# Kernel tuning notes

Measured on AMD Instinct MI355X. Metric: run time of the kernel, lower is better.

Reference implementation:

```python
import jax, jax.numpy as jnp
import numpy as np

ALPHA = 50.0  # softmax temperature from __init__
EPS = 1e-12   # torch F.normalize eps


def _l2norm(v, axis):
    return v / jnp.maximum(jnp.linalg.norm(v, axis=axis, keepdims=True), EPS)


def setup_inputs() -> dict:
    key = jax.random.key(0)
    k1, k2 = jax.random.split(key)
    N, C, H, W, K = 64, 512, 32, 32, 64
    x = jax.random.normal(k1, (N, C, H, W), jnp.float32)
    # conv.weight after _init_params has shape (dim, num_clusters) = (C, K)
    conv_weight = jax.random.normal(k2, (C, K), jnp.float32) * 0.05
    conv_bias = jnp.zeros((K,), jnp.float32)
    return {"x": x, "conv_weight": conv_weight, "conv_bias": conv_bias}


def reference(x, conv_weight, conv_bias):
    N, C, H, W = x.shape
    HW = H * W
    # normalize_input=True: L2 normalize over channel dim
    xn = _l2norm(x, axis=1)
    xf = xn.reshape(N, C, HW)                      # [N, C, HW]
    # column-normalized projection weight (F.normalize(conv.weight, dim=0))
    Wn = _l2norm(conv_weight, axis=0)              # [C, K]
    # soft assignment logits: x^T Wn -> stored as [N, K, HW]
    sa_logits = jnp.einsum('nch,ck->nkh', xf, Wn)  # [N, K, HW]
    soft_assign = jax.nn.softmax((sa_logits + conv_bias[None, :, None]) * ALPHA, axis=1)
    # VLAD via two batched contractions instead of the [N,K,C,HW] residual tensor:
    # sum_h a[n,k,h] * (x[n,:,h] - W[:,k]) = (a @ x^T)[n,k,:] - (sum_h a) * W[:,k]
    vlad = jnp.einsum('nkh,nch->nkc', soft_assign, xf) \
         - soft_assign.sum(-1)[..., None] * conv_weight.T[None]   # [N, K, C]
    vlad = _l2norm(vlad, axis=2).reshape(N, -1)    # intra-norm + flatten -> [N, K*C]
    feature = jnp.transpose(xf, (0, 2, 1))         # [N, HW, C]
    return (vlad, sa_logits, feature)
```

## Files before the change

kernel.cpp:

```cpp
#include <hip/hip_runtime.h>
#include <math.h>

#define N_   64
#define C_   512
#define HW_  1024
#define K_   64
#define ALPHA_ 50.0f
#define EPS_  1e-12f

#define OUT_VLAD 0
#define OUT_SA   2097152
#define OUT_FEAT 6291456

#define WSB_WT    0
#define WSB_WNTB  131072
#define WSB_INVN  196608
#define WSB_A     458752
#define WSB_SUMA  8847360
#define WSB_PART  8863744
#define PART_ELEMS 2097152

typedef __attribute__((ext_vector_type(8))) __bf16 bf16x8;
typedef __attribute__((ext_vector_type(4))) float f32x4;
typedef __attribute__((ext_vector_type(8))) unsigned short ushort8v;

__device__ inline unsigned short f2bf(float f) {
    unsigned int u = __builtin_bit_cast(unsigned int, f);
    u = (u + 0x7FFFu + ((u >> 16) & 1u)) >> 16;
    return (unsigned short)u;
}
__device__ inline float bf2f(unsigned short h) {
    unsigned int u = ((unsigned int)h) << 16;
    return __builtin_bit_cast(float, u);
}
__device__ inline f32x4 mfma16(const unsigned short* pa, const unsigned short* pb, f32x4 c) {
    bf16x8 a = *(const bf16x8*)pa;
    bf16x8 b = *(const bf16x8*)pb;
    return __builtin_amdgcn_mfma_f32_16x16x32_bf16(a, b, c, 0, 0, 0);
}

__global__ __launch_bounds__(256) void k1_weights(const float* __restrict__ W,
                                                  float* __restrict__ wT,
                                                  unsigned short* __restrict__ wnTb) {
    int k = blockIdx.x;
    int t = threadIdx.x;
    __shared__ float red[256];
    float s = 0.f;
    for (int c = t; c < C_; c += 256) { float w = W[c * K_ + k]; s += w * w; }
    red[t] = s;
    __syncthreads();
    for (int st = 128; st > 0; st >>= 1) {
        if (t < st) red[t] += red[t + st];
        __syncthreads();
    }
    float inv = 1.f / fmaxf(sqrtf(red[0]), EPS_);
    for (int c = t; c < C_; c += 256) {
        float w = W[c * K_ + k];
        wT[k * C_ + c]   = w;
        wnTb[k * C_ + c] = f2bf(w * inv);
    }
}

__global__ __launch_bounds__(256) void k2_normfeat(const float* __restrict__ x,
                                                   float* __restrict__ out,
                                                   float* __restrict__ invn) {
    float* feat = out + OUT_FEAT;
    int b   = blockIdx.x;
    int n   = b >> 6;
    int hw0 = (b & 63) << 4;
    int t   = threadIdx.x;
    __shared__ float Xs[C_ * 17 + 256 + 16];
    float* red = Xs + C_ * 17;
    float* nrm = red + 256;
    const float* xn = x + (long)n * C_ * HW_;
    for (int j = 0; j < 32; ++j) {
        int idx = j * 256 + t;
        int c = idx >> 4, p = idx & 15;
        Xs[c * 17 + p] = xn[c * HW_ + hw0 + p];
    }
    __syncthreads();
    {
        int p = t & 15, cg = t >> 4;
        float s = 0.f;
        for (int j = 0; j < 32; ++j) {
            float v = Xs[(cg + 16 * j) * 17 + p];
            s += v * v;
        }
        red[t] = s;
    }
    __syncthreads();
    if (t < 16) {
        float s = 0.f;
        for (int g = 0; g < 16; ++g) s += red[g * 16 + t];
        float iv = 1.f / fmaxf(sqrtf(s), EPS_);
        nrm[t] = iv;
        invn[(long)n * HW_ + hw0 + t] = iv;
    }
    __syncthreads();
    float* frow = feat + ((long)n * HW_ + hw0) * C_;
    for (int p = 0; p < 16; ++p) {
        float iv = nrm[p];
        frow[(long)p * C_ + t]       = Xs[t * 17 + p] * iv;
        frow[(long)p * C_ + t + 256] = Xs[(t + 256) * 17 + p] * iv;
    }
}

#define K3PITCH 136
__global__ __launch_bounds__(256, 4) void k3_sa(const float* __restrict__ feat,
                                                const unsigned short* __restrict__ wnTb,
                                                const float* __restrict__ bias,
                                                float* __restrict__ sa,
                                                unsigned short* __restrict__ Ab) {
    __shared__ alignas(16) unsigned short sm[128 * K3PITCH + 64 * K3PITCH];
    unsigned short* Fsh = sm;
    unsigned short* Wsh = sm + 128 * K3PITCH;
    float* Ls = (float*)sm;
    float* Bz = Ls + 8448;
    float* Zm = Ls + 8512;
    float* Iv = Ls + 8640;

    int b   = blockIdx.x;
    int n   = b >> 3;
    int hw0 = (b & 7) << 7;
    int t   = threadIdx.x;
    int l   = t & 63, w = t >> 6;
    int mr  = l & 15, q = l >> 4;

    f32x4 acc[2][4];
#pragma unroll
    for (int i = 0; i < 2; ++i)
#pragma unroll
        for (int j = 0; j < 4; ++j) acc[i][j] = (f32x4){0.f, 0.f, 0.f, 0.f};

    const float* fb = feat + ((long)n * HW_ + hw0) * C_;
    for (int ch = 0; ch < 4; ++ch) {
        int c0 = ch * 128;
        __syncthreads();
#pragma unroll
        for (int j = 0; j < 8; ++j) {
            int idx = j * 256 + t;
            int row = idx >> 4, sg = idx & 15;
            const float* src = fb + (long)row * C_ + c0 + sg * 8;
            float4 v0 = *(const float4*)src;
            float4 v1 = *(const float4*)(src + 4);
            ushort8v pk;
            pk[0] = f2bf(v0.x); pk[1] = f2bf(v0.y); pk[2] = f2bf(v0.z); pk[3] = f2bf(v0.w);
            pk[4] = f2bf(v1.x); pk[5] = f2bf(v1.y); pk[6] = f2bf(v1.z); pk[7] = f2bf(v1.w);
            *(ushort8v*)(Fsh + row * K3PITCH + sg * 8) = pk;
        }
#pragma unroll
        for (int j = 0; j < 4; ++j) {
            int idx = j * 256 + t;
            int row = idx >> 4, sg = idx & 15;
            *(uint4*)(Wsh + row * K3PITCH + sg * 8) =
                *(const uint4*)(wnTb + row * C_ + c0 + sg * 8);
        }
        __syncthreads();
#pragma unroll
        for (int ks = 0; ks < 4; ++ks) {
            int ko = ks * 32 + q * 8;
            const unsigned short* ap0 = Fsh + (w * 32 + mr) * K3PITCH + ko;
            const unsigned short* ap1 = Fsh + (w * 32 + 16 + mr) * K3PITCH + ko;
#pragma unroll
            for (int j = 0; j < 4; ++j) {
                const unsigned short* bp = Wsh + (j * 16 + mr) * K3PITCH + ko;
                acc[0][j] = mfma16(ap0, bp, acc[0][j]);
                acc[1][j] = mfma16(ap1, bp, acc[1][j]);
            }
        }
    }
    __syncthreads();
#pragma unroll
    for (int i = 0; i < 2; ++i)
#pragma unroll
        for (int j = 0; j < 4; ++j)
#pragma unroll
            for (int r = 0; r < 4; ++r)
                Ls[(j * 16 + mr) * 132 + w * 32 + i * 16 + q * 4 + r] = acc[i][j][r];
    if (t < 64) Bz[t] = bias[t];
    __syncthreads();
    if (t < 128) {
        int p = t;
        float mx = -1e30f;
        for (int kc = 0; kc < 64; ++kc) {
            float z = (Ls[kc * 132 + p] + Bz[kc]) * ALPHA_;
            mx = fmaxf(mx, z);
        }
        float s = 0.f;
        for (int kc = 0; kc < 64; ++kc) {
            float z = (Ls[kc * 132 + p] + Bz[kc]) * ALPHA_;
            s += __expf(z - mx);
        }
        Zm[p] = mx;
        Iv[p] = 1.f / s;
    }
    __syncthreads();
    float* sab = sa + (long)n * K_ * HW_ + hw0;
    unsigned short* Arow = Ab + (long)n * K_ * HW_ + hw0;
#pragma unroll
    for (int j = 0; j < 32; ++j) {
        int idx = j * 256 + t;
        int kc = idx >> 7, p = idx & 127;
        float v = Ls[kc * 132 + p];
        sab[(long)kc * HW_ + p] = v;
        float z = (v + Bz[kc]) * ALPHA_;
        Arow[(long)kc * HW_ + p] = f2bf(__expf(z - Zm[p]) * Iv[p]);
    }
}

__global__ __launch_bounds__(256) void k3b_suma(const unsigned short* __restrict__ Ab,
                                                float* __restrict__ sumA) {
    int b = blockIdx.x, t = threadIdx.x;
    int wv = t >> 6, l = t & 63;
    int row = b * 4 + wv;
    const unsigned int* ar = (const unsigned int*)(Ab + (long)row * HW_);
    float s = 0.f;
#pragma unroll
    for (int i = 0; i < 8; ++i) {
        unsigned int u = ar[i * 64 + l];
        s += bf2f((unsigned short)(u & 0xFFFF)) + bf2f((unsigned short)(u >> 16));
    }
#pragma unroll
    for (int off = 32; off > 0; off >>= 1) s += __shfl_down(s, off, 64);
    if (l == 0) sumA[row] = s;
}

#define K4PITCH 72
__global__ __launch_bounds__(256, 4) void k4_vlad(const float* __restrict__ x,
                                                  const float* __restrict__ invn,
                                                  const unsigned short* __restrict__ Ab,
                                                  float* __restrict__ part) {
    __shared__ float invs[512];
    __shared__ alignas(16) unsigned short Ash[64 * K4PITCH];
    __shared__ alignas(16) unsigned short Fsh[128 * K4PITCH];
    int b  = blockIdx.x;
    int n  = b >> 3;
    int r  = b & 7;
    int ct = r & 3, hh = r >> 2;
    int c_off = ct * 128, h_base = hh * 512;
    int t = threadIdx.x;
    int l = t & 63, w = t >> 6;
    int mr = l & 15, q = l >> 4;
    int kcb = (w >> 1) * 32, cb = (w & 1) * 64;

    invs[t]       = invn[(long)n * HW_ + h_base + t];
    invs[t + 256] = invn[(long)n * HW_ + h_base + 256 + t];

    f32x4 acc[2][4];
#pragma unroll
    for (int i = 0; i < 2; ++i)
#pragma unroll
        for (int j = 0; j < 4; ++j) acc[i][j] = (f32x4){0.f, 0.f, 0.f, 0.f};

    const unsigned short* Abase = Ab + (long)n * K_ * HW_ + h_base;
    const float* xbase = x + ((long)n * C_ + c_off) * HW_ + h_base;

    for (int ch = 0; ch < 8; ++ch) {
        int h0 = ch * 64;
        __syncthreads();
#pragma unroll
        for (int j = 0; j < 2; ++j) {
            int idx = j * 256 + t;
            int row = idx >> 3, sg = idx & 7;
            *(uint4*)(Ash + row * K4PITCH + sg * 8) =
                *(const uint4*)(Abase + (long)row * HW_ + h0 + sg * 8);
        }
#pragma unroll
        for (int j = 0; j < 4; ++j) {
            int idx = j * 256 + t;
            int row = idx >> 3, sg = idx & 7;
            const float* src = xbase + (long)row * HW_ + h0 + sg * 8;
            float4 v0 = *(const float4*)src;
            float4 v1 = *(const float4*)(src + 4);
            const float* iv = invs + h0 + sg * 8;
            ushort8v pk;
            pk[0] = f2bf(v0.x * iv[0]); pk[1] = f2bf(v0.y * iv[1]);
            pk[2] = f2bf(v0.z * iv[2]); pk[3] = f2bf(v0.w * iv[3]);
            pk[4] = f2bf(v1.x * iv[4]); pk[5] = f2bf(v1.y * iv[5]);
            pk[6] = f2bf(v1.z * iv[6]); pk[7] = f2bf(v1.w * iv[7]);
            *(ushort8v*)(Fsh + row * K4PITCH + sg * 8) = pk;
        }
        __syncthreads();
#pragma unroll
        for (int ks = 0; ks < 2; ++ks) {
            int ko = ks * 32 + q * 8;
            const unsigned short* ap0 = Ash + (kcb + mr) * K4PITCH + ko;
            const unsigned short* ap1 = Ash + (kcb + 16 + mr) * K4PITCH + ko;
#pragma unroll
            for (int j = 0; j < 4; ++j) {
                const unsigned short* bp = Fsh + (cb + j * 16 + mr) * K4PITCH + ko;
                acc[0][j] = mfma16(ap0, bp, acc[0][j]);
                acc[1][j] = mfma16(ap1, bp, acc[1][j]);
            }
        }
    }
    float* pb = part + (long)hh * PART_ELEMS + (long)n * K_ * C_ + c_off;
#pragma unroll
    for (int i = 0; i < 2; ++i)
#pragma unroll
        for (int j = 0; j < 4; ++j)
#pragma unroll
            for (int r = 0; r < 4; ++r) {
                int kc = kcb + i * 16 + q * 4 + r;
                int c  = cb + j * 16 + mr;
                pb[(long)kc * C_ + c] = acc[i][j][r];
            }
}

__global__ __launch_bounds__(256) void k5_norm(const float* __restrict__ part,
                                               const float* __restrict__ sumA,
                                               const float* __restrict__ wT,
                                               float* __restrict__ vlad) {
    __shared__ float red[256];
    int row = blockIdx.x;
    int kc  = row & 63;
    int t   = threadIdx.x;
    float sA = sumA[row];
    long base = (long)row * C_;
    float v0, v1;
    {
        int c = t;
        float s = part[base + c] + part[PART_ELEMS + base + c];
        v0 = s - sA * wT[kc * C_ + c];
    }
    {
        int c = t + 256;
        float s = part[base + c] + part[PART_ELEMS + base + c];
        v1 = s - sA * wT[kc * C_ + c];
    }
    red[t] = v0 * v0 + v1 * v1;
    __syncthreads();
    for (int st = 128; st > 0; st >>= 1) {
        if (t < st) red[t] += red[t + st];
        __syncthreads();
    }
    float inv = 1.f / fmaxf(sqrtf(red[0]), EPS_);
    vlad[base + t]       = v0 * inv;
    vlad[base + t + 256] = v1 * inv;
}

extern "C" void kernel_launch(void* const* d_in, const int* in_sizes, int n_in,
                              void* d_out, int out_size, void* d_ws, size_t ws_size,
                              hipStream_t stream) {
    const float* x    = (const float*)d_in[0];
    const float* W    = (const float*)d_in[1];
    const float* bias = (const float*)d_in[2];
    float* out = (float*)d_out;
    char* wsb  = (char*)d_ws;

    float* wT           = (float*)(wsb + WSB_WT);
    unsigned short* wnTb = (unsigned short*)(wsb + WSB_WNTB);
    float* invn         = (float*)(wsb + WSB_INVN);
    unsigned short* Ab  = (unsigned short*)(wsb + WSB_A);
    float* sumA         = (float*)(wsb + WSB_SUMA);
    float* part         = (float*)(wsb + WSB_PART);

    float* vlad = out + OUT_VLAD;
    float* sa   = out + OUT_SA;
    float* feat = out + OUT_FEAT;

    hipLaunchKernelGGL(k1_weights, dim3(64),   dim3(256), 0, stream, W, wT, wnTb);
    hipLaunchKernelGGL(k2_normfeat, dim3(4096), dim3(256), 0, stream, x, out, invn);
    hipLaunchKernelGGL(k3_sa,      dim3(512),  dim3(256), 0, stream, feat, wnTb, bias, sa, Ab);
    hipLaunchKernelGGL(k3b_suma,   dim3(1024), dim3(256), 0, stream, Ab, sumA);
    hipLaunchKernelGGL(k4_vlad,    dim3(512),  dim3(256), 0, stream, x, invn, Ab, part);
    hipLaunchKernelGGL(k5_norm,    dim3(4096), dim3(256), 0, stream, part, sumA, wT, vlad);
}
```

Measured before the change: 353.9 us.

## Fuse soft-assignment sum into k3, halve tiles in k3/k4 for more blocks

Removes the separate k3b_suma kernel: k3_sa now writes per-tile partial row sums of the soft assignment, and k5 reduces the 16 partials per row. k3 and k4 use half-size tiles so each grid has 1024 blocks, meant to improve occupancy across the CUs. The softmax is also spread over all 256 threads instead of 128. The trade-off is more redundant weight and tile loads per block, plus extra syncs.

New measurement: 344.5 us. 1.03x faster.

```diff
diff --git a/kernel.cpp b/kernel.cpp
--- a/kernel.cpp
+++ b/kernel.cpp
@@ -16,8 +16,8 @@
 #define WSB_WNTB  131072
 #define WSB_INVN  196608
 #define WSB_A     458752
-#define WSB_SUMA  8847360
-#define WSB_PART  8863744
+#define WSB_SAP   8847360
+#define WSB_PART  9109504
 #define PART_ELEMS 2097152
 
 typedef __attribute__((ext_vector_type(8))) __bf16 bf16x8;
@@ -110,34 +110,36 @@
                                                 const unsigned short* __restrict__ wnTb,
                                                 const float* __restrict__ bias,
                                                 float* __restrict__ sa,
-                                                unsigned short* __restrict__ Ab) {
-    __shared__ alignas(16) unsigned short sm[128 * K3PITCH + 64 * K3PITCH];
+                                                unsigned short* __restrict__ Ab,
+                                                float* __restrict__ sumA_part) {
+    __shared__ alignas(16) unsigned short sm[64 * K3PITCH + 64 * K3PITCH];
     unsigned short* Fsh = sm;
-    unsigned short* Wsh = sm + 128 * K3PITCH;
+    unsigned short* Wsh = sm + 64 * K3PITCH;
     float* Ls = (float*)sm;
-    float* Bz = Ls + 8448;
-    float* Zm = Ls + 8512;
-    float* Iv = Ls + 8640;
-
-    int b   = blockIdx.x;
-    int n   = b >> 3;
-    int hw0 = (b & 7) << 7;
-    int t   = threadIdx.x;
-    int l   = t & 63, w = t >> 6;
-    int mr  = l & 15, q = l >> 4;
-
-    f32x4 acc[2][4];
-#pragma unroll
-    for (int i = 0; i < 2; ++i)
-#pragma unroll
-        for (int j = 0; j < 4; ++j) acc[i][j] = (f32x4){0.f, 0.f, 0.f, 0.f};
+    float* Bz = Ls + 64 * 66;
+    float* Zm = Bz + 64;
+    float* Iv = Zm + 64;
+    float* Rm = Iv + 64;
+    float* Rs = Rm + 256;
+
+    int b    = blockIdx.x;
+    int n    = b >> 4;
+    int tile = b & 15;
+    int hw0  = tile << 6;
+    int t    = threadIdx.x;
+    int l    = t & 63, w = t >> 6;
+    int mr   = l & 15, q = l >> 4;
+
+    f32x4 acc[4];
+#pragma unroll
+    for (int j = 0; j < 4; ++j) acc[j] = (f32x4){0.f, 0.f, 0.f, 0.f};
 
     const float* fb = feat + ((long)n * HW_ + hw0) * C_;
     for (int ch = 0; ch < 4; ++ch) {
         int c0 = ch * 128;
         __syncthreads();
 #pragma unroll
-        for (int j = 0; j < 8; ++j) {
+        for (int j = 0; j < 4; ++j) {
             int idx = j * 256 + t;
             int row = idx >> 4, sg = idx & 15;
             const float* src = fb + (long)row * C_ + c0 + sg * 8;
@@ -159,70 +161,67 @@
 #pragma unroll
         for (int ks = 0; ks < 4; ++ks) {
             int ko = ks * 32 + q * 8;
-            const unsigned short* ap0 = Fsh + (w * 32 + mr) * K3PITCH + ko;
-            const unsigned short* ap1 = Fsh + (w * 32 + 16 + mr) * K3PITCH + ko;
+            const unsigned short* ap = Fsh + (w * 16 + mr) * K3PITCH + ko;
 #pragma unroll
             for (int j = 0; j < 4; ++j) {
                 const unsigned short* bp = Wsh + (j * 16 + mr) * K3PITCH + ko;
-                acc[0][j] = mfma16(ap0, bp, acc[0][j]);
-                acc[1][j] = mfma16(ap1, bp, acc[1][j]);
+                acc[j] = mfma16(ap, bp, acc[j]);
             }
         }
     }
     __syncthreads();
 #pragma unroll
-    for (int i = 0; i < 2; ++i)
-#pragma unroll
-        for (int j = 0; j < 4; ++j)
-#pragma unroll
-            for (int r = 0; r < 4; ++r)
-                Ls[(j * 16 + mr) * 132 + w * 32 + i * 16 + q * 4 + r] = acc[i][j][r];
+    for (int j = 0; j < 4; ++j)
+#pragma unroll
+        for (int r = 0; r < 4; ++r)
+            Ls[(j * 16 + mr) * 66 + w * 16 + q * 4 + r] = acc[j][r];
     if (t < 64) Bz[t] = bias[t];
     __syncthreads();
-    if (t < 128) {
-        int p = t;
+    {
+        int p = t & 63, g = t >> 6;
         float mx = -1e30f;
-        for (int kc = 0; kc < 64; ++kc) {
-            float z = (Ls[kc * 132 + p] + Bz[kc]) * ALPHA_;
+#pragma unroll
+        for (int kk = 0; kk < 16; ++kk) {
+            int kc = g * 16 + kk;
+            float z = (Ls[kc * 66 + p] + Bz[kc]) * ALPHA_;
             mx = fmaxf(mx, z);
         }
+        Rm[g * 64 + p] = mx;
+        __syncthreads();
+        float M = fmaxf(fmaxf(Rm[p], Rm[64 + p]), fmaxf(Rm[128 + p], Rm[192 + p]));
         float s = 0.f;
-        for (int kc = 0; kc < 64; ++kc) {
-            float z = (Ls[kc * 132 + p] + Bz[kc]) * ALPHA_;
-            s += __expf(z - mx);
-        }
-        Zm[p] = mx;
-        Iv[p] = 1.f / s;
+#pragma unroll
+        for (int kk = 0; kk < 16; ++kk) {
+            int kc = g * 16 + kk;
+            float z = (Ls[kc * 66 + p] + Bz[kc]) * ALPHA_;
+            s += __expf(z - M);
+        }
+        Rs[g * 64 + p] = s;
+        __syncthreads();
+        if (g == 0) {
+            Zm[p] = M;
+            Iv[p] = 1.f / (Rs[p] + Rs[64 + p] + Rs[128 + p] + Rs[192 + p]);
+        }
     }
     __syncthreads();
     float* sab = sa + (long)n * K_ * HW_ + hw0;
     unsigned short* Arow = Ab + (long)n * K_ * HW_ + hw0;
 #pragma unroll
-    for (int j = 0; j < 32; ++j) {
+    for (int j = 0; j < 16; ++j) {
         int idx = j * 256 + t;
-        int kc = idx >> 7, p = idx & 127;
-        float v = Ls[kc * 132 + p];
+        int kc = idx >> 6, p = idx & 63;
+        float v = Ls[kc * 66 + p];
         sab[(long)kc * HW_ + p] = v;
-        float z = (v + Bz[kc]) * ALPHA_;
-        Arow[(long)kc * HW_ + p] = f2bf(__expf(z - Zm[p]) * Iv[p]);
-    }
-}
-
-__global__ __launch_bounds__(256) void k3b_suma(const unsigned short* __restrict__ Ab,
-                                                float* __restrict__ sumA) {
-    int b = blockIdx.x, t = threadIdx.x;
-    int wv = t >> 6, l = t & 63;
-    int row = b * 4 + wv;
-    const unsigned int* ar = (const unsigned int*)(Ab + (long)row * HW_);
-    float s = 0.f;
-#pragma unroll
-    for (int i = 0; i < 8; ++i) {
-        unsigned int u = ar[i * 64 + l];
-        s += bf2f((unsigned short)(u & 0xFFFF)) + bf2f((unsigned short)(u >> 16));
-    }
-#pragma unroll
-    for (int off = 32; off > 0; off >>= 1) s += __shfl_down(s, off, 64);
-    if (l == 0) sumA[row] = s;
+        float a = __expf((v + Bz[kc]) * ALPHA_ - Zm[p]) * Iv[p];
+        Arow[(long)kc * HW_ + p] = f2bf(a);
+        Ls[kc * 66 + p] = a;
+    }
+    __syncthreads();
+    if (t < 64) {
+        float s = 0.f;
+        for (int p2 = 0; p2 < 64; ++p2) s += Ls[t * 66 + p2];
+        sumA_part[((long)n * 16 + tile) * 64 + t] = s;
+    }
 }
 
 #define K4PITCH 72
@@ -232,25 +231,26 @@
                                                   float* __restrict__ part) {
     __shared__ float invs[512];
     __shared__ alignas(16) unsigned short Ash[64 * K4PITCH];
-    __shared__ alignas(16) unsigned short Fsh[128 * K4PITCH];
+    __shared__ alignas(16) unsigned short Fsh[64 * K4PITCH];
     int b  = blockIdx.x;
-    int n  = b >> 3;
-    int r  = b & 7;
-    int ct = r & 3, hh = r >> 2;
-    int c_off = ct * 128, h_base = hh * 512;
+    int n  = b >> 4;
+    int r  = b & 15;
+    int c_off  = (r & 7) * 64;
+    int hh     = r >> 3;
+    int h_base = hh * 512;
     int t = threadIdx.x;
     int l = t & 63, w = t >> 6;
     int mr = l & 15, q = l >> 4;
-    int kcb = (w >> 1) * 32, cb = (w & 1) * 64;
+    int kcb = (w >> 1) * 32, cb = (w & 1) * 32;
 
     invs[t]       = invn[(long)n * HW_ + h_base + t];
     invs[t + 256] = invn[(long)n * HW_ + h_base + 256 + t];
 
-    f32x4 acc[2][4];
+    f32x4 acc[2][2];
 #pragma unroll
     for (int i = 0; i < 2; ++i)
 #pragma unroll
-        for (int j = 0; j < 4; ++j) acc[i][j] = (f32x4){0.f, 0.f, 0.f, 0.f};
+        for (int j = 0; j < 2; ++j) acc[i][j] = (f32x4){0.f, 0.f, 0.f, 0.f};
 
     const unsigned short* Abase = Ab + (long)n * K_ * HW_ + h_base;
     const float* xbase = x + ((long)n * C_ + c_off) * HW_ + h_base;
@@ -266,7 +266,7 @@
                 *(const uint4*)(Abase + (long)row * HW_ + h0 + sg * 8);
         }
 #pragma unroll
-        for (int j = 0; j < 4; ++j) {
+        for (int j = 0; j < 2; ++j) {
             int idx = j * 256 + t;
             int row = idx >> 3, sg = idx & 7;
             const float* src = xbase + (long)row * HW_ + h0 + sg * 8;
@@ -287,7 +287,7 @@
             const unsigned short* ap0 = Ash + (kcb + mr) * K4PITCH + ko;
             const unsigned short* ap1 = Ash + (kcb + 16 + mr) * K4PITCH + ko;
 #pragma unroll
-            for (int j = 0; j < 4; ++j) {
+            for (int j = 0; j < 2; ++j) {
                 const unsigned short* bp = Fsh + (cb + j * 16 + mr) * K4PITCH + ko;
                 acc[0][j] = mfma16(ap0, bp, acc[0][j]);
                 acc[1][j] = mfma16(ap1, bp, acc[1][j]);
@@ -298,24 +298,30 @@
 #pragma unroll
     for (int i = 0; i < 2; ++i)
 #pragma unroll
-        for (int j = 0; j < 4; ++j)
-#pragma unroll
-            for (int r = 0; r < 4; ++r) {
-                int kc = kcb + i * 16 + q * 4 + r;
+        for (int j = 0; j < 2; ++j)
+#pragma unroll
+            for (int rr = 0; rr < 4; ++rr) {
+                int kc = kcb + i * 16 + q * 4 + rr;
                 int c  = cb + j * 16 + mr;
-                pb[(long)kc * C_ + c] = acc[i][j][r];
+                pb[(long)kc * C_ + c] = acc[i][j][rr];
             }
 }
 
 __global__ __launch_bounds__(256) void k5_norm(const float* __restrict__ part,
-                                               const float* __restrict__ sumA,
+                                               const float* __restrict__ sumA_part,
                                                const float* __restrict__ wT,
                                                float* __restrict__ vlad) {
     __shared__ float red[256];
+    __shared__ float sred[16];
     int row = blockIdx.x;
     int kc  = row & 63;
+    int n   = row >> 6;
     int t   = threadIdx.x;
-    float sA = sumA[row];
+    if (t < 16) sred[t] = sumA_part[((long)n * 16 + t) * 64 + kc];
+    __syncthreads();
+    float sA = 0.f;
+#pragma unroll
+    for (int i = 0; i < 16; ++i) sA += sred[i];
     long base = (long)row * C_;
     float v0, v1;
     {
@@ -348,21 +354,20 @@
     float* out = (float*)d_out;
     char* wsb  = (char*)d_ws;
 
-    float* wT           = (float*)(wsb + WSB_WT);
+    float* wT            = (float*)(wsb + WSB_WT);
     unsigned short* wnTb = (unsigned short*)(wsb + WSB_WNTB);
-    float* invn         = (float*)(wsb + WSB_INVN);
-    unsigned short* Ab  = (unsigned short*)(wsb + WSB_A);
-    float* sumA         = (float*)(wsb + WSB_SUMA);
-    float* part         = (float*)(wsb + WSB_PART);
+    float* invn          = (float*)(wsb + WSB_INVN);
+    unsigned short* Ab   = (unsigned short*)(wsb + WSB_A);
+    float* sumA_part     = (float*)(wsb + WSB_SAP);
+    float* part          = (float*)(wsb + WSB_PART);
 
     float* vlad = out + OUT_VLAD;
     float* sa   = out + OUT_SA;
     float* feat = out + OUT_FEAT;
 
-    hipLaunchKernelGGL(k1_weights, dim3(64),   dim3(256), 0, stream, W, wT, wnTb);
+    hipLaunchKernelGGL(k1_weights,  dim3(64),   dim3(256), 0, stream, W, wT, wnTb);
     hipLaunchKernelGGL(k2_normfeat, dim3(4096), dim3(256), 0, stream, x, out, invn);
-    hipLaunchKernelGGL(k3_sa,      dim3(512),  dim3(256), 0, stream, feat, wnTb, bias, sa, Ab);
-    hipLaunchKernelGGL(k3b_suma,   dim3(1024), dim3(256), 0, stream, Ab, sumA);
-    hipLaunchKernelGGL(k4_vlad,    dim3(512),  dim3(256), 0, stream, x, invn, Ab, part);
-    hipLaunchKernelGGL(k5_norm,    dim3(4096), dim3(256), 0, stream, part, sumA, wT, vlad);
-}
+    hipLaunchKernelGGL(k3_sa,       dim3(1024), dim3(256), 0, stream, feat, wnTb, bias, sa, Ab, sumA_part);
+    hipLaunchKernelGGL(k4_vlad,     dim3(1024), dim3(256), 0, stream, x, invn, Ab, part);
+    hipLaunchKernelGGL(k5_norm,     dim3(4096), dim3(256), 0, stream, part, sumA_part, wT, vlad);
+}
```
